# Performance work log

Measured on AMD Instinct MI355X. Metric: run time of the kernel, lower is better.

The kernel has to match this reference:

```python
import jax, jax.numpy as jnp
import numpy as np
from math import log

GROUP_SIZE, NUM_CLIPS, C = 8, 64, 4


def _static_tables(N, C, group_size):
    # Replicates get_2d_mask from the original repo (2D-TAN sparse pattern)
    num_group = int(log(N / (2 * group_size), 2)) + 1
    pooling_counts = [2 * group_size - 1] + [group_size] * (num_group - 1)
    mask = np.zeros((N, N), dtype=np.float32)
    mask[np.arange(N), np.arange(N)] = 1.0
    stride, offset = 1, 0
    for cnt in pooling_counts:
        for _ in range(cnt):
            offset += stride
            i = np.arange(0, N - offset, stride)
            j = np.arange(offset, N, stride)
            mask[i, j] = 1.0
        stride *= 2
    # Segment boundaries SS/EE per (c, s, e): mean over x[:, :, SS:EE]
    SS = np.zeros((C, N, N), dtype=np.int32)
    EE = np.ones((C, N, N), dtype=np.int32)  # dummy count=1 for e<s (masked out)
    for s in range(N):
        for e in range(s, N):
            if e + 1 - s < C:
                SS[:, s, e] = s
                EE[:, s, e] = e + 1
            else:
                idx = np.linspace(s, e + 1, C + 1).astype(np.int64)  # matches torch.linspace(...).long()
                SS[:, s, e] = idx[:C]
                EE[:, s, e] = idx[1:]
    EE = np.maximum(EE, SS + 1)  # guard against zero counts in masked-out cells
    return SS, EE, mask


def setup_inputs() -> dict:
    key = jax.random.key(0)
    x = jax.random.normal(key, (16, 512, NUM_CLIPS), dtype=jnp.float32)
    return {"x": x}


def reference(x):
    SS_np, EE_np, mask_np = _static_tables(NUM_CLIPS, C, GROUP_SIZE)
    SS = jnp.asarray(SS_np)            # [C, N, N]
    EE = jnp.asarray(EE_np)            # [C, N, N]
    mask2d = jnp.asarray(mask_np)      # [N, N]
    B, D, N = x.shape
    # Exclusive prefix sum along clips: P[k] = sum(x[..., :k]); P has length N+1.
    P = jnp.concatenate([jnp.zeros((B, D, 1), dtype=x.dtype), jnp.cumsum(x, axis=2)], axis=2)
    # Segment sums via two gathers: [B, D, C, N, N]
    sums = P[:, :, EE] - P[:, :, SS]
    counts = (EE - SS).astype(x.dtype)  # [C, N, N], broadcasts
    map2d = sums / counts
    return map2d * mask2d  # mask2d broadcasts over [B, D, C, N, N]
```

## Files before the change

kernel.cpp:

```cpp
#include <hip/hip_runtime.h>


#define NN 64
#define COUT 4

__global__ __launch_bounds__(256)
void smin_pool_kernel(const float* __restrict__ x, float* __restrict__ out) {
    __shared__ float P[NN + 1];

    const int bd = blockIdx.x;
    const int t  = threadIdx.x;

    if (t < 64) {
        float v = x[(size_t)bd * NN + t];
        #pragma unroll
        for (int off = 1; off < 64; off <<= 1) {
            float u = __shfl_up(v, off, 64);
            if (t >= off) v += u;
        }
        P[t + 1] = v;
        if (t == 0) P[0] = 0.0f;
    }
    __syncthreads();

    float4* out4 = (float4*)(out + (size_t)bd * (COUT * NN * NN));

    #pragma unroll
    for (int k = 0; k < 16; ++k) {
        const int idx4 = t + k * 256;
        const int c  = idx4 >> 10;
        const int s  = (idx4 >> 4) & 63;
        const int e0 = (idx4 & 15) << 2;

        float4 r;
        float* rp = &r.x;
        #pragma unroll
        for (int j = 0; j < 4; ++j) {
            const int e = e0 + j;
            const int d = e - s;
            bool m;
            if (d < 0)        m = false;
            else if (d <= 15) m = true;
            else if (d <= 31) m = (d & 1) && !(s & 1);
            else              m = ((d & 3) == 3) && !(s & 3);

            float val = 0.0f;
            if (m) {
                const int L = d + 1;
                int ss, ee;
                if (L < COUT) { ss = s; ee = e + 1; }
                else {
                    ss = s + ((c * L) >> 2);
                    ee = s + (((c + 1) * L) >> 2);
                }
                if (ee < ss + 1) ee = ss + 1;
                val = (P[ee] - P[ss]) / (float)(ee - ss);
            }
            rp[j] = val;
        }
        out4[idx4] = r;
    }
}

extern "C" void kernel_launch(void* const* d_in, const int* in_sizes, int n_in,
                              void* d_out, int out_size, void* d_ws, size_t ws_size,
                              hipStream_t stream) {
    const float* x = (const float*)d_in[0];
    float* out = (float*)d_out;
    const int BD = in_sizes[0] / NN;
    smin_pool_kernel<<<BD, 256, 0, stream>>>(x, out);
}
```

Before: 523.4 us.

## Precompute packed segment-bound and reciprocal lookup table in a separate kernel

Adds a small kernel that builds, in workspace, a 64K-entry table packing the start index, end index and an fp16 reciprocal of the count for every (c, s, e) output cell. The main kernel then reads one uint4 of table entries per float4 output, does two shared-memory loads and a multiply, and drops the per-element mask logic and float division. The table is rebuilt on every call and should stay in cache. Storing the reciprocal in fp16 loses precision and may exceed the accuracy tolerance. An extra kernel launch is added.

```diff
diff --git a/kernel.cpp b/kernel.cpp
--- a/kernel.cpp
+++ b/kernel.cpp
@@ -1,13 +1,46 @@
 #include <hip/hip_runtime.h>
+#include <hip/hip_fp16.h>
 
 
 #define NN 64
 #define COUT 4
+#define TAB_N (COUT * NN * NN)
 
 __global__ __launch_bounds__(256)
-void smin_pool_kernel(const float* __restrict__ x, float* __restrict__ out) {
+void smin_build_table(unsigned int* __restrict__ tab) {
+    const int idx = blockIdx.x * 256 + threadIdx.x;
+    const int c = idx >> 12;
+    const int s = (idx >> 6) & 63;
+    const int e = idx & 63;
+    const int d = e - s;
+    bool m;
+    if (d < 0)        m = false;
+    else if (d <= 15) m = true;
+    else if (d <= 31) m = (d & 1) && !(s & 1);
+    else              m = ((d & 3) == 3) && !(s & 3);
+
+    unsigned int packed = 0u;
+    if (m) {
+        const int L = d + 1;
+        int ss, ee;
+        if (L < COUT) { ss = s; ee = e + 1; }
+        else {
+            ss = s + ((c * L) >> 2);
+            ee = s + (((c + 1) * L) >> 2);
+        }
+        if (ee < ss + 1) ee = ss + 1;
+        const float rcp = 1.0f / (float)(ee - ss);
+        const unsigned short h = __half_as_ushort(__float2half(rcp));
+        packed = (unsigned)ss | ((unsigned)ee << 8) | ((unsigned)h << 16);
+    }
+    tab[idx] = packed;
+}
+
+__global__ __launch_bounds__(256)
+void smin_pool_kernel(const float* __restrict__ x,
+                      const uint4* __restrict__ tab4,
+                      float* __restrict__ out) {
     __shared__ float P[NN + 1];
-
     const int bd = blockIdx.x;
     const int t  = threadIdx.x;
 
@@ -23,40 +56,32 @@
     }
     __syncthreads();
 
-    float4* out4 = (float4*)(out + (size_t)bd * (COUT * NN * NN));
+    float4* out4 = (float4*)(out + (size_t)bd * TAB_N);
 
     #pragma unroll
     for (int k = 0; k < 16; ++k) {
         const int idx4 = t + k * 256;
-        const int c  = idx4 >> 10;
-        const int s  = (idx4 >> 4) & 63;
-        const int e0 = (idx4 & 15) << 2;
-
+        const uint4 tv = tab4[idx4];
         float4 r;
-        float* rp = &r.x;
-        #pragma unroll
-        for (int j = 0; j < 4; ++j) {
-            const int e = e0 + j;
-            const int d = e - s;
-            bool m;
-            if (d < 0)        m = false;
-            else if (d <= 15) m = true;
-            else if (d <= 31) m = (d & 1) && !(s & 1);
-            else              m = ((d & 3) == 3) && !(s & 3);
-
-            float val = 0.0f;
-            if (m) {
-                const int L = d + 1;
-                int ss, ee;
-                if (L < COUT) { ss = s; ee = e + 1; }
-                else {
-                    ss = s + ((c * L) >> 2);
-                    ee = s + (((c + 1) * L) >> 2);
-                }
-                if (ee < ss + 1) ee = ss + 1;
-                val = (P[ee] - P[ss]) / (float)(ee - ss);
-            }
-            rp[j] = val;
+        {
+            const unsigned v = tv.x;
+            r.x = (P[(v >> 8) & 255] - P[v & 255]) *
+                  __half2float(__ushort_as_half((unsigned short)(v >> 16)));
+        }
+        {
+            const unsigned v = tv.y;
+            r.y = (P[(v >> 8) & 255] - P[v & 255]) *
+                  __half2float(__ushort_as_half((unsigned short)(v >> 16)));
+        }
+        {
+            const unsigned v = tv.z;
+            r.z = (P[(v >> 8) & 255] - P[v & 255]) *
+                  __half2float(__ushort_as_half((unsigned short)(v >> 16)));
+        }
+        {
+            const unsigned v = tv.w;
+            r.w = (P[(v >> 8) & 255] - P[v & 255]) *
+                  __half2float(__ushort_as_half((unsigned short)(v >> 16)));
         }
         out4[idx4] = r;
     }
@@ -67,6 +92,9 @@
                               hipStream_t stream) {
     const float* x = (const float*)d_in[0];
     float* out = (float*)d_out;
+    unsigned int* tab = (unsigned int*)d_ws;
     const int BD = in_sizes[0] / NN;
-    smin_pool_kernel<<<BD, 256, 0, stream>>>(x, out);
+
+    smin_build_table<<<TAB_N / 256, 256, 0, stream>>>(tab);
+    smin_pool_kernel<<<BD, 256, 0, stream>>>(x, (const uint4*)d_ws, out);
 }
```

Measured after the change: 526.4 us. No clear change (+0.6%).
